# Optimization experiments

Hardware: AMD Instinct MI355X
Metric: run time of the kernel (lower is better)

The kernel has to match this reference:

```python
import jax, jax.numpy as jnp
import numpy as np

B, N, A, D = 16, 256, 64, 256


def setup_inputs() -> dict:
    key = jax.random.key(0)
    ks = jax.random.split(key, 9)
    s = 1.0 / np.sqrt(D)
    return {
        "cc_embeds": jax.random.normal(ks[0], (B, N, D), jnp.float32),
        "anchor_embeds": jax.random.normal(ks[1], (B, N, A, D), jnp.float32),
        "sims": jax.random.normal(ks[2], (B, N, A), jnp.float32),
        "Wq": jax.random.normal(ks[3], (D, D), jnp.float32) * s,
        "bq": jax.random.normal(ks[4], (D,), jnp.float32) * s,
        "Wk": jax.random.normal(ks[5], (D, D), jnp.float32) * s,
        "bk": jax.random.normal(ks[6], (D,), jnp.float32) * s,
        "Wv": jax.random.normal(ks[7], (D, D), jnp.float32) * s,
        "bv": jax.random.normal(ks[8], (D,), jnp.float32) * s,
    }


def reference(cc_embeds, anchor_embeds, sims, Wq, bq, Wk, bk, Wv, bv):
    # Linear projections (torch nn.Linear: x @ W.T + b)
    Q = cc_embeds @ Wq.T + bq                    # [B, N, D]
    K = anchor_embeds @ Wk.T + bk                # [B, N, A, D]
    V = anchor_embeds @ Wv.T + bv                # [B, N, A, D]
    scale = 1.0 / jnp.sqrt(jnp.asarray(D, Q.dtype))
    scores = jnp.einsum('bnd,bnad->bna', Q, K) * scale  # [B, N, A]
    adj = scores + sims                          # additive similarity bias
    # conditional softmax: rows whose raw sum == 0 are passed through unchanged
    nonzero = jnp.sum(adj, axis=-1, keepdims=True) != 0
    probs = jnp.where(nonzero, jax.nn.softmax(adj, axis=-1), adj)
    out = jnp.einsum('bna,bnad->bnd', probs, V)  # [B, N, D]
    return out[:, :, None, :]                    # match torch output [B, N, 1, D]
```

## Files before the change

kernel.cpp:

```cpp
#include <hip/hip_runtime.h>
#include <hip/hip_bf16.h>


typedef float f4 __attribute__((ext_vector_type(4)));

__device__ __forceinline__ float bcast_lane(float x, int lane) {
  return __int_as_float(__builtin_amdgcn_readlane(__float_as_int(x), lane));
}

__global__ __launch_bounds__(256) void k1_prep(
    const float* __restrict__ Wq, const float* __restrict__ bq,
    const float* __restrict__ Wk, const float* __restrict__ bk,
    const float* __restrict__ Wv,
    float* __restrict__ M, float* __restrict__ rvec, float* __restrict__ uvec,
    float* __restrict__ s0, float* __restrict__ WvT) {
  __shared__ float colL[256];
  __shared__ float pr[256];
  __shared__ float tile[64][65];
  const int tid = threadIdx.x;
  const int bid = blockIdx.x;
  if (bid < 256) {
    colL[tid] = Wq[tid * 256 + bid];
    __syncthreads();
    float acc = 0.f;
#pragma unroll 4
    for (int d = 0; d < 256; ++d) acc += colL[d] * Wk[d * 256 + tid];
    M[bid * 256 + tid] = acc;
  } else if (bid == 256) {
    colL[tid] = bq[tid];
    __syncthreads();
    float acc = 0.f;
#pragma unroll 4
    for (int d = 0; d < 256; ++d) acc += colL[d] * Wk[d * 256 + tid];
    rvec[tid] = acc;
  } else if (bid == 257) {
    colL[tid] = bk[tid];
    pr[tid] = bq[tid] * bk[tid];
    __syncthreads();
    float acc = 0.f;
#pragma unroll 4
    for (int d = 0; d < 256; ++d) acc += Wq[d * 256 + tid] * colL[d];
    uvec[tid] = acc;
    if (tid == 0) {
      float s = 0.f;
      for (int d = 0; d < 256; ++d) s += pr[d];
      s0[0] = s;
    }
  } else {
    const int tb = bid - 258, bi = tb >> 2, bj = tb & 3;
#pragma unroll
    for (int k = 0; k < 16; ++k) {
      int idx = k * 256 + tid;
      int r = idx >> 6, cL = idx & 63;
      tile[r][cL] = Wv[(bi * 64 + r) * 256 + bj * 64 + cL];
    }
    __syncthreads();
#pragma unroll
    for (int k = 0; k < 16; ++k) {
      int idx = k * 256 + tid;
      int r = idx >> 6, cL = idx & 63;
      WvT[(bj * 64 + r) * 256 + bi * 64 + cL] = tile[cL][r];
    }
  }
}

__global__ __launch_bounds__(256) void k2_proj(
    const float* __restrict__ cc, const float* __restrict__ M,
    const float* __restrict__ rvec, const float* __restrict__ uvec,
    const float* __restrict__ s0p,
    float* __restrict__ tmat, float* __restrict__ cvec) {
  __shared__ __align__(16) float pOut[4][8][256];
  __shared__ float cpart[4][8];
  const int tid = threadIdx.x;
  const int w = tid >> 6, L = tid & 63;
  const int i0 = blockIdx.x * 8;
  const int e0 = w * 64;
  float ccreg[8];
#pragma unroll
  for (int r = 0; r < 8; ++r) ccreg[r] = cc[(size_t)(i0 + r) * 256 + e0 + L];
  float uvl = uvec[e0 + L];
  f4 acc[8] = {};
#pragma unroll 8
  for (int ee = 0; ee < 64; ++ee) {
    f4 m = *(const f4*)(M + (size_t)(e0 + ee) * 256 + 4 * L);
#pragma unroll
    for (int r = 0; r < 8; ++r) {
      float cv = bcast_lane(ccreg[r], ee);
      acc[r].x += cv * m.x; acc[r].y += cv * m.y;
      acc[r].z += cv * m.z; acc[r].w += cv * m.w;
    }
  }
#pragma unroll
  for (int r = 0; r < 8; ++r) *(f4*)&pOut[w][r][4 * L] = acc[r];
#pragma unroll
  for (int r = 0; r < 8; ++r) {
    float pc = ccreg[r] * uvl;
#pragma unroll
    for (int off = 32; off >= 1; off >>= 1) pc += __shfl_xor(pc, off, 64);
    if (L == 0) cpart[w][r] = pc;
  }
  __syncthreads();
  float rv = rvec[tid];
#pragma unroll
  for (int r = 0; r < 8; ++r) {
    float s = pOut[0][r][tid] + pOut[1][r][tid] + pOut[2][r][tid] + pOut[3][r][tid];
    tmat[(size_t)(i0 + r) * 256 + tid] = s + rv;
  }
  if (tid < 8)
    cvec[i0 + tid] = cpart[0][tid] + cpart[1][tid] + cpart[2][tid] + cpart[3][tid] + s0p[0];
}

__global__ __launch_bounds__(256) void k3_attn(
    const float* __restrict__ anchor, const float* __restrict__ sims,
    const float* __restrict__ tmat, const float* __restrict__ cvec,
    float* __restrict__ wout, float* __restrict__ psum) {
  __shared__ float sL[64];
  __shared__ float pL[64];
  __shared__ __align__(16) float pW[4 * 256];
  __shared__ float psh;
  const int i = blockIdx.x;
  const int tid = threadIdx.x;
  const int lane = tid & 63, w = tid >> 6;

  const f4* g4 = (const f4*)(anchor + (size_t)i * 16384);
  f4 v[16];
#pragma unroll
  for (int k = 0; k < 16; ++k) v[k] = __builtin_nontemporal_load(g4 + k * 256 + tid);
  const f4 t4 = ((const f4*)(tmat + (size_t)i * 256))[lane];

#pragma unroll
  for (int k = 0; k < 16; ++k) {
    float s = v[k].x * t4.x + v[k].y * t4.y + v[k].z * t4.z + v[k].w * t4.w;
#pragma unroll
    for (int off = 32; off >= 1; off >>= 1) s += __shfl_xor(s, off, 64);
    if (lane == 0) sL[k * 4 + w] = s;
  }
  __syncthreads();
  if (tid < 64) {
    float adj = (sL[tid] + cvec[i]) * 0.0625f + sims[(size_t)i * 64 + tid];
    float ssum = adj, smax = adj;
    for (int off = 32; off >= 1; off >>= 1) {
      ssum += __shfl_xor(ssum, off, 64);
      smax = fmaxf(smax, __shfl_xor(smax, off, 64));
    }
    float p;
    if (ssum != 0.f) {
      p = expf(adj - smax);
      float z = p;
      for (int off = 32; off >= 1; off >>= 1) z += __shfl_xor(z, off, 64);
      p = p / z;
    } else {
      p = adj;
    }
    float ps = p;
    for (int off = 32; off >= 1; off >>= 1) ps += __shfl_xor(ps, off, 64);
    pL[tid] = p;
    if (tid == 0) psh = ps;
  }
  __syncthreads();
  f4 acc = {0.f, 0.f, 0.f, 0.f};
#pragma unroll
  for (int k = 0; k < 16; ++k) {
    float p = pL[k * 4 + w];
    acc.x += p * v[k].x; acc.y += p * v[k].y;
    acc.z += p * v[k].z; acc.w += p * v[k].w;
  }
  *(f4*)(pW + w * 256 + 4 * lane) = acc;
  __syncthreads();
  float val = pW[tid] + pW[256 + tid] + pW[512 + tid] + pW[768 + tid];
  wout[(size_t)i * 256 + tid] = val;
  if (tid == 0) psum[i] = psh;
}

__global__ __launch_bounds__(256) void k4_out(
    const float* __restrict__ wmat, const float* __restrict__ WvT,
    const float* __restrict__ bv, const float* __restrict__ psum,
    float* __restrict__ out) {
  __shared__ __align__(16) float pOut[4][8][256];
  const int tid = threadIdx.x;
  const int w = tid >> 6, L = tid & 63;
  const int i0 = blockIdx.x * 8;
  const int e0 = w * 64;
  float wreg[8];
#pragma unroll
  for (int r = 0; r < 8; ++r) wreg[r] = wmat[(size_t)(i0 + r) * 256 + e0 + L];
  f4 acc[8] = {};
#pragma unroll 8
  for (int ee = 0; ee < 64; ++ee) {
    f4 m = *(const f4*)(WvT + (size_t)(e0 + ee) * 256 + 4 * L);
#pragma unroll
    for (int r = 0; r < 8; ++r) {
      float cv = bcast_lane(wreg[r], ee);
      acc[r].x += cv * m.x; acc[r].y += cv * m.y;
      acc[r].z += cv * m.z; acc[r].w += cv * m.w;
    }
  }
#pragma unroll
  for (int r = 0; r < 8; ++r) *(f4*)&pOut[w][r][4 * L] = acc[r];
  __syncthreads();
  float b = bv[tid];
#pragma unroll
  for (int r = 0; r < 8; ++r) {
    float s = pOut[0][r][tid] + pOut[1][r][tid] + pOut[2][r][tid] + pOut[3][r][tid];
    out[(size_t)(i0 + r) * 256 + tid] = s + b * psum[i0 + r];
  }
}

extern "C" void kernel_launch(void* const* d_in, const int* in_sizes, int n_in,
                              void* d_out, int out_size, void* d_ws, size_t ws_size,
                              hipStream_t stream) {
  const float* cc     = (const float*)d_in[0];
  const float* anchor = (const float*)d_in[1];
  const float* sims   = (const float*)d_in[2];
  const float* Wq     = (const float*)d_in[3];
  const float* bq     = (const float*)d_in[4];
  const float* Wk     = (const float*)d_in[5];
  const float* bk     = (const float*)d_in[6];
  const float* Wv     = (const float*)d_in[7];
  const float* bv     = (const float*)d_in[8];
  float* out = (float*)d_out;
  float* ws  = (float*)d_ws;

  float* M    = ws;
  float* WvT  = ws + 65536;
  float* rvec = ws + 131072;
  float* uvec = ws + 131328;
  float* s0   = ws + 131584;
  float* cvec = ws + 131840;
  float* psum = ws + 135936;
  float* tmat = ws + 140032;
  float* wmat = tmat + 1048576;

  k1_prep<<<274, 256, 0, stream>>>(Wq, bq, Wk, bk, Wv, M, rvec, uvec, s0, WvT);
  k2_proj<<<512, 256, 0, stream>>>(cc, M, rvec, uvec, s0, tmat, cvec);
  k3_attn<<<4096, 256, 0, stream>>>(anchor, sims, tmat, cvec, wmat, psum);
  k4_out<<<512, 256, 0, stream>>>(wmat, WvT, bv, psum, out);
}
```

Before: 410.7 us.

## Fuse projection, attention and output kernels into one per-8-row kernel

Merges the query projection, per-row attention softmax and value output projection into a single kernel that handles 8 rows per block, keeping intermediates in shared memory instead of global buffers. Anchor rows are processed serially with the next row's loads issued before the current reduction finishes. This removes intermediate global traffic and two launches, but cuts the grid from 4096 to 512 blocks for the bandwidth-heavy anchor streaming, which reduces memory-level parallelism.

Result: no change. 414.4 us (+0.9%).

```diff
diff --git a/kernel.cpp b/kernel.cpp
--- a/kernel.cpp
+++ b/kernel.cpp
@@ -64,145 +64,151 @@
   }
 }
 
-__global__ __launch_bounds__(256) void k2_proj(
-    const float* __restrict__ cc, const float* __restrict__ M,
-    const float* __restrict__ rvec, const float* __restrict__ uvec,
-    const float* __restrict__ s0p,
-    float* __restrict__ tmat, float* __restrict__ cvec) {
+__global__ __launch_bounds__(256) void k_main(
+    const float* __restrict__ cc, const float* __restrict__ anchor,
+    const float* __restrict__ sims,
+    const float* __restrict__ M, const float* __restrict__ rvec,
+    const float* __restrict__ uvec, const float* __restrict__ s0p,
+    const float* __restrict__ WvT, const float* __restrict__ bv,
+    float* __restrict__ out) {
   __shared__ __align__(16) float pOut[4][8][256];
+  __shared__ __align__(16) float t8[8][256];
+  __shared__ __align__(16) float w8[8][256];
   __shared__ float cpart[4][8];
+  __shared__ float c8[8];
+  __shared__ float ps8[8];
+  __shared__ float sL[64];
+  __shared__ float pL[64];
   const int tid = threadIdx.x;
   const int w = tid >> 6, L = tid & 63;
   const int i0 = blockIdx.x * 8;
   const int e0 = w * 64;
+
   float ccreg[8];
 #pragma unroll
   for (int r = 0; r < 8; ++r) ccreg[r] = cc[(size_t)(i0 + r) * 256 + e0 + L];
   float uvl = uvec[e0 + L];
-  f4 acc[8] = {};
+  {
+    f4 acc[8] = {};
 #pragma unroll 8
-  for (int ee = 0; ee < 64; ++ee) {
-    f4 m = *(const f4*)(M + (size_t)(e0 + ee) * 256 + 4 * L);
+    for (int ee = 0; ee < 64; ++ee) {
+      f4 m = *(const f4*)(M + (size_t)(e0 + ee) * 256 + 4 * L);
+#pragma unroll
+      for (int r = 0; r < 8; ++r) {
+        float cv = bcast_lane(ccreg[r], ee);
+        acc[r].x += cv * m.x; acc[r].y += cv * m.y;
+        acc[r].z += cv * m.z; acc[r].w += cv * m.w;
+      }
+    }
+#pragma unroll
+    for (int r = 0; r < 8; ++r) *(f4*)&pOut[w][r][4 * L] = acc[r];
 #pragma unroll
     for (int r = 0; r < 8; ++r) {
-      float cv = bcast_lane(ccreg[r], ee);
-      acc[r].x += cv * m.x; acc[r].y += cv * m.y;
-      acc[r].z += cv * m.z; acc[r].w += cv * m.w;
-    }
-  }
-#pragma unroll
-  for (int r = 0; r < 8; ++r) *(f4*)&pOut[w][r][4 * L] = acc[r];
-#pragma unroll
+      float pc = ccreg[r] * uvl;
+#pragma unroll
+      for (int off = 32; off >= 1; off >>= 1) pc += __shfl_xor(pc, off, 64);
+      if (L == 0) cpart[w][r] = pc;
+    }
+  }
+
+  const f4* g4 = (const f4*)(anchor + (size_t)i0 * 16384);
+  f4 v[16];
+#pragma unroll
+  for (int k = 0; k < 16; ++k) v[k] = __builtin_nontemporal_load(g4 + k * 256 + tid);
+
+  __syncthreads();
+  {
+    float rv = rvec[tid];
+#pragma unroll
+    for (int r = 0; r < 8; ++r)
+      t8[r][tid] = pOut[0][r][tid] + pOut[1][r][tid] + pOut[2][r][tid] +
+                   pOut[3][r][tid] + rv;
+    if (tid < 8)
+      c8[tid] = cpart[0][tid] + cpart[1][tid] + cpart[2][tid] + cpart[3][tid] + s0p[0];
+  }
+  __syncthreads();
+
+  float* pW = &pOut[0][0][0];
   for (int r = 0; r < 8; ++r) {
-    float pc = ccreg[r] * uvl;
-#pragma unroll
-    for (int off = 32; off >= 1; off >>= 1) pc += __shfl_xor(pc, off, 64);
-    if (L == 0) cpart[w][r] = pc;
-  }
-  __syncthreads();
-  float rv = rvec[tid];
-#pragma unroll
-  for (int r = 0; r < 8; ++r) {
-    float s = pOut[0][r][tid] + pOut[1][r][tid] + pOut[2][r][tid] + pOut[3][r][tid];
-    tmat[(size_t)(i0 + r) * 256 + tid] = s + rv;
-  }
-  if (tid < 8)
-    cvec[i0 + tid] = cpart[0][tid] + cpart[1][tid] + cpart[2][tid] + cpart[3][tid] + s0p[0];
-}
-
-__global__ __launch_bounds__(256) void k3_attn(
-    const float* __restrict__ anchor, const float* __restrict__ sims,
-    const float* __restrict__ tmat, const float* __restrict__ cvec,
-    float* __restrict__ wout, float* __restrict__ psum) {
-  __shared__ float sL[64];
-  __shared__ float pL[64];
-  __shared__ __align__(16) float pW[4 * 256];
-  __shared__ float psh;
-  const int i = blockIdx.x;
-  const int tid = threadIdx.x;
-  const int lane = tid & 63, w = tid >> 6;
-
-  const f4* g4 = (const f4*)(anchor + (size_t)i * 16384);
-  f4 v[16];
-#pragma unroll
-  for (int k = 0; k < 16; ++k) v[k] = __builtin_nontemporal_load(g4 + k * 256 + tid);
-  const f4 t4 = ((const f4*)(tmat + (size_t)i * 256))[lane];
-
-#pragma unroll
-  for (int k = 0; k < 16; ++k) {
-    float s = v[k].x * t4.x + v[k].y * t4.y + v[k].z * t4.z + v[k].w * t4.w;
-#pragma unroll
-    for (int off = 32; off >= 1; off >>= 1) s += __shfl_xor(s, off, 64);
-    if (lane == 0) sL[k * 4 + w] = s;
-  }
-  __syncthreads();
-  if (tid < 64) {
-    float adj = (sL[tid] + cvec[i]) * 0.0625f + sims[(size_t)i * 64 + tid];
-    float ssum = adj, smax = adj;
-    for (int off = 32; off >= 1; off >>= 1) {
-      ssum += __shfl_xor(ssum, off, 64);
-      smax = fmaxf(smax, __shfl_xor(smax, off, 64));
-    }
-    float p;
-    if (ssum != 0.f) {
-      p = expf(adj - smax);
-      float z = p;
-      for (int off = 32; off >= 1; off >>= 1) z += __shfl_xor(z, off, 64);
-      p = p / z;
-    } else {
-      p = adj;
-    }
-    float ps = p;
-    for (int off = 32; off >= 1; off >>= 1) ps += __shfl_xor(ps, off, 64);
-    pL[tid] = p;
-    if (tid == 0) psh = ps;
-  }
-  __syncthreads();
-  f4 acc = {0.f, 0.f, 0.f, 0.f};
-#pragma unroll
-  for (int k = 0; k < 16; ++k) {
-    float p = pL[k * 4 + w];
-    acc.x += p * v[k].x; acc.y += p * v[k].y;
-    acc.z += p * v[k].z; acc.w += p * v[k].w;
-  }
-  *(f4*)(pW + w * 256 + 4 * lane) = acc;
-  __syncthreads();
-  float val = pW[tid] + pW[256 + tid] + pW[512 + tid] + pW[768 + tid];
-  wout[(size_t)i * 256 + tid] = val;
-  if (tid == 0) psum[i] = psh;
-}
-
-__global__ __launch_bounds__(256) void k4_out(
-    const float* __restrict__ wmat, const float* __restrict__ WvT,
-    const float* __restrict__ bv, const float* __restrict__ psum,
-    float* __restrict__ out) {
-  __shared__ __align__(16) float pOut[4][8][256];
-  const int tid = threadIdx.x;
-  const int w = tid >> 6, L = tid & 63;
-  const int i0 = blockIdx.x * 8;
-  const int e0 = w * 64;
-  float wreg[8];
-#pragma unroll
-  for (int r = 0; r < 8; ++r) wreg[r] = wmat[(size_t)(i0 + r) * 256 + e0 + L];
-  f4 acc[8] = {};
+    const f4 t4 = *(const f4*)&t8[r][4 * L];
+#pragma unroll
+    for (int k = 0; k < 16; ++k) {
+      float s = v[k].x * t4.x + v[k].y * t4.y + v[k].z * t4.z + v[k].w * t4.w;
+#pragma unroll
+      for (int off = 32; off >= 1; off >>= 1) s += __shfl_xor(s, off, 64);
+      if (L == 0) sL[k * 4 + w] = s;
+    }
+    __syncthreads();
+    if (tid < 64) {
+      float adj = (sL[tid] + c8[r]) * 0.0625f + sims[(size_t)(i0 + r) * 64 + tid];
+      float ssum = adj, smax = adj;
+#pragma unroll
+      for (int off = 32; off >= 1; off >>= 1) {
+        ssum += __shfl_xor(ssum, off, 64);
+        smax = fmaxf(smax, __shfl_xor(smax, off, 64));
+      }
+      float p;
+      if (ssum != 0.f) {
+        p = expf(adj - smax);
+        float z = p;
+#pragma unroll
+        for (int off = 32; off >= 1; off >>= 1) z += __shfl_xor(z, off, 64);
+        p = p / z;
+      } else {
+        p = adj;
+      }
+      float ps = p;
+#pragma unroll
+      for (int off = 32; off >= 1; off >>= 1) ps += __shfl_xor(ps, off, 64);
+      pL[tid] = p;
+      if (tid == 0) ps8[r] = ps;
+    }
+    __syncthreads();
+    f4 acc = {0.f, 0.f, 0.f, 0.f};
+#pragma unroll
+    for (int k = 0; k < 16; ++k) {
+      float p = pL[k * 4 + w];
+      acc.x += p * v[k].x; acc.y += p * v[k].y;
+      acc.z += p * v[k].z; acc.w += p * v[k].w;
+    }
+    if (r < 7) {
+      const f4* g4n = (const f4*)(anchor + (size_t)(i0 + r + 1) * 16384);
+#pragma unroll
+      for (int k = 0; k < 16; ++k)
+        v[k] = __builtin_nontemporal_load(g4n + k * 256 + tid);
+    }
+    *(f4*)&pW[w * 256 + 4 * L] = acc;
+    __syncthreads();
+    w8[r][tid] = pW[tid] + pW[256 + tid] + pW[512 + tid] + pW[768 + tid];
+  }
+  __syncthreads();
+
+  {
+    float wreg[8];
+#pragma unroll
+    for (int r = 0; r < 8; ++r) wreg[r] = w8[r][e0 + L];
+    f4 acc[8] = {};
 #pragma unroll 8
-  for (int ee = 0; ee < 64; ++ee) {
-    f4 m = *(const f4*)(WvT + (size_t)(e0 + ee) * 256 + 4 * L);
+    for (int ee = 0; ee < 64; ++ee) {
+      f4 m = *(const f4*)(WvT + (size_t)(e0 + ee) * 256 + 4 * L);
+#pragma unroll
+      for (int r = 0; r < 8; ++r) {
+        float cv = bcast_lane(wreg[r], ee);
+        acc[r].x += cv * m.x; acc[r].y += cv * m.y;
+        acc[r].z += cv * m.z; acc[r].w += cv * m.w;
+      }
+    }
+#pragma unroll
+    for (int r = 0; r < 8; ++r) *(f4*)&pOut[w][r][4 * L] = acc[r];
+  }
+  __syncthreads();
+  {
+    float b = bv[tid];
 #pragma unroll
     for (int r = 0; r < 8; ++r) {
-      float cv = bcast_lane(wreg[r], ee);
-      acc[r].x += cv * m.x; acc[r].y += cv * m.y;
-      acc[r].z += cv * m.z; acc[r].w += cv * m.w;
-    }
-  }
-#pragma unroll
-  for (int r = 0; r < 8; ++r) *(f4*)&pOut[w][r][4 * L] = acc[r];
-  __syncthreads();
-  float b = bv[tid];
-#pragma unroll
-  for (int r = 0; r < 8; ++r) {
-    float s = pOut[0][r][tid] + pOut[1][r][tid] + pOut[2][r][tid] + pOut[3][r][tid];
-    out[(size_t)(i0 + r) * 256 + tid] = s + b * psum[i0 + r];
+      float s = pOut[0][r][tid] + pOut[1][r][tid] + pOut[2][r][tid] + pOut[3][r][tid];
+      out[(size_t)(i0 + r) * 256 + tid] = s + b * ps8[r];
+    }
   }
 }
 
@@ -226,13 +232,7 @@
   float* rvec = ws + 131072;
   float* uvec = ws + 131328;
   float* s0   = ws + 131584;
-  float* cvec = ws + 131840;
-  float* psum = ws + 135936;
-  float* tmat = ws + 140032;
-  float* wmat = tmat + 1048576;
 
   k1_prep<<<274, 256, 0, stream>>>(Wq, bq, Wk, bk, Wv, M, rvec, uvec, s0, WvT);
-  k2_proj<<<512, 256, 0, stream>>>(cc, M, rvec, uvec, s0, tmat, cvec);
-  k3_attn<<<4096, 256, 0, stream>>>(anchor, sims, tmat, cvec, wmat, psum);
-  k4_out<<<512, 256, 0, stream>>>(wmat, WvT, bv, psum, out);
-}
+  k_main<<<512, 256, 0, stream>>>(cc, anchor, sims, M, rvec, uvec, s0, WvT, bv, out);
+}
```
